# Kernel tuning notes

Hardware: AMD Instinct MI355X
Metric: run time of the kernel (lower is better)

The kernel has to match this reference:

```python
import jax, jax.numpy as jnp
import numpy as np

N_NODES = 100000


def gcn_conv(x, W, b, src, dst, ew, n):
    """PyG GCNConv with edge_weight: add self-loops (weight 1), symmetric norm,
    linear transform, scatter-add aggregation, bias."""
    h = x @ W                                   # [N, F_out]
    # degree includes the self-loop weight of 1 per node
    deg = jnp.zeros((n,), dtype=x.dtype).at[dst].add(ew) + 1.0
    dinv = jax.lax.rsqrt(deg)                   # deg > 0 always (self-loop)
    norm = dinv[src] * ew * dinv[dst]           # [E]
    agg = jax.ops.segment_sum(h[src] * norm[:, None], dst, num_segments=n)
    # self-loop contribution: norm_ii = dinv[i]^2 * 1
    agg = agg + h * (dinv * dinv)[:, None]
    return agg + b


def setup_inputs() -> dict:
    key = jax.random.key(0)
    ks = jax.random.split(key, 9)
    N, E, F_in, F_h, F_out = N_NODES, 1600000, 128, 64, 10
    x = jax.random.normal(ks[0], (N, F_in), dtype=jnp.float32)
    edge_index = jax.random.randint(ks[1], (2, E), 0, N, dtype=jnp.int64)
    edge_weight = jax.random.uniform(ks[2], (E,), dtype=jnp.float32)
    def glorot(k, fi, fo):
        s = jnp.sqrt(6.0 / (fi + fo))
        return jax.random.uniform(k, (fi, fo), minval=-s, maxval=s, dtype=jnp.float32)
    return {
        "x": x,
        "edge_index": edge_index,
        "edge_weight": edge_weight,
        "W1": glorot(ks[3], F_in, F_h), "b1": jnp.zeros((F_h,), jnp.float32),
        "W2": glorot(ks[4], F_h, F_h), "b2": jnp.zeros((F_h,), jnp.float32),
        "Wfc": glorot(ks[5], F_h, F_out), "bfc": jnp.zeros((F_out,), jnp.float32),
    }


def reference(x, edge_index, edge_weight, W1, b1, W2, b2, Wfc, bfc):
    n = x.shape[0]
    src, dst = edge_index[0], edge_index[1]
    h = gcn_conv(x, W1, b1, src, dst, edge_weight, n)
    h = jax.nn.relu(h)
    h = gcn_conv(h, W2, b2, src, dst, edge_weight, n)
    h = jax.nn.relu(h)
    return h @ Wfc + bfc
```

## Files before the change

kernel.cpp:

```cpp
#include <hip/hip_runtime.h>

static constexpr int F_IN  = 128;
static constexpr int F_H   = 64;
static constexpr int F_OUT = 10;

static constexpr int NPB_SHIFT = 9;
static constexpr int NPB = 1 << NPB_SHIFT;
static constexpr int MAXC = 256;
static constexpr int EPB = 2048;

__device__ __forceinline__ unsigned short f2bf(float f) {
    unsigned u = __float_as_uint(f);
    return (unsigned short)((u + 0x7fff + ((u >> 16) & 1)) >> 16);
}
__device__ __forceinline__ float bf_lo(unsigned u) { return __uint_as_float(u << 16); }
__device__ __forceinline__ float bf_hi(unsigned u) { return __uint_as_float(u & 0xffff0000u); }

__global__ __launch_bounds__(64) void k_detect(const unsigned long long* __restrict__ u,
                                               int* __restrict__ flag) {
    unsigned long long v = u[threadIdx.x];
    int hz = ((v >> 32) == 0ull) ? 1 : 0;
    int all64 = __all(hz);
    if (threadIdx.x == 0) flag[0] = all64;
}

__device__ __forceinline__ int load_idx(const void* ein, bool f64, long i) {
    return f64 ? (int)((const long long*)ein)[i] : ((const int*)ein)[i];
}

__global__ __launch_bounds__(256) void k_part1(const void* __restrict__ ein,
                                               const float* __restrict__ ew,
                                               const int* __restrict__ flag,
                                               int* __restrict__ gcur,
                                               unsigned long long* __restrict__ packed,
                                               int E, int NC, int cap) {
    __shared__ int lcnt[MAXC];
    __shared__ int lofs[MAXC];
    int tid = threadIdx.x;
    if (tid < NC) lcnt[tid] = 0;
    __syncthreads();
    bool f = flag[0];
    int base = blockIdx.x * EPB;
#pragma unroll
    for (int j = 0; j < EPB / 256; ++j) {
        int e = base + j * 256 + tid;
        if (e < E) {
            int d = load_idx(ein, f, (long)E + e);
            atomicAdd(&lcnt[d >> NPB_SHIFT], 1);
        }
    }
    __syncthreads();
    if (tid < NC) {
        int c = lcnt[tid];
        lofs[tid] = c ? atomicAdd(&gcur[tid], c) : 0;
        lcnt[tid] = 0;
    }
    __syncthreads();
#pragma unroll
    for (int j = 0; j < EPB / 256; ++j) {
        int e = base + j * 256 + tid;
        if (e < E) {
            int s = load_idx(ein, f, e);
            int d = load_idx(ein, f, (long)E + e);
            unsigned int wb = __float_as_uint(ew[e]);
            int b = d >> NPB_SHIFT;
            int pos = lofs[b] + atomicAdd(&lcnt[b], 1);
            if (pos < cap) {
                unsigned long long u = (unsigned long long)wb
                                     | ((unsigned long long)(unsigned)s << 32)
                                     | ((unsigned long long)(unsigned)(d & (NPB - 1)) << 49);
                packed[(long)b * cap + pos] = u;
            }
        }
    }
}

__global__ __launch_bounds__(256) void k_chist(const unsigned long long* __restrict__ packed,
                                               const int* __restrict__ gcur,
                                               int* __restrict__ rp,
                                               int* __restrict__ pbt,
                                               float* __restrict__ dinv,
                                               int N, int cap) {
    __shared__ int   lc[NPB];
    __shared__ float ld[NPB];
    __shared__ int   sm[256];
    int b = blockIdx.x, tid = threadIdx.x;
#pragma unroll
    for (int i = tid; i < NPB; i += 256) { lc[i] = 0; ld[i] = 0.0f; }
    __syncthreads();
    int cnt = gcur[b];
    const unsigned long long* pk = packed + (long)b * cap;
    for (int p = tid; p < cnt; p += 256) {
        unsigned long long u = pk[p];
        int dl = (int)(u >> 49);
        atomicAdd(&lc[dl], 1);
        atomicAdd(&ld[dl], __uint_as_float((unsigned int)u));
    }
    __syncthreads();
    int c0 = lc[tid * 2], c1 = lc[tid * 2 + 1];
    int p0 = (c0 + 15) & ~15, p1 = (c1 + 15) & ~15;
    int s = p0 + p1;
    sm[tid] = s;
    __syncthreads();
    for (int off = 1; off < 256; off <<= 1) {
        int v = 0;
        if (tid >= off) v = sm[tid - off];
        __syncthreads();
        sm[tid] += v;
        __syncthreads();
    }
    int excl = sm[tid] - s;
    int n0 = b << NPB_SHIFT;
    int node0 = n0 + tid * 2, node1 = node0 + 1;
    if (node0 < N) {
        rp[node0]   = excl;
        dinv[node0] = rsqrtf(ld[tid * 2] + 1.0f);
    }
    if (node1 < N) {
        rp[node1]   = excl + p0;
        dinv[node1] = rsqrtf(ld[tid * 2 + 1] + 1.0f);
    }
    if (tid == 255) pbt[b] = sm[255];
}

__global__ __launch_bounds__(256) void k_scanP(const int* __restrict__ pbt,
                                               int* __restrict__ pbase,
                                               int* __restrict__ rp, int NC, int N) {
    __shared__ int sm[256];
    int tid = threadIdx.x;
    int c = (tid < NC) ? pbt[tid] : 0;
    sm[tid] = c;
    __syncthreads();
    for (int off = 1; off < 256; off <<= 1) {
        int v = 0;
        if (tid >= off) v = sm[tid - off];
        __syncthreads();
        sm[tid] += v;
        __syncthreads();
    }
    if (tid < NC) pbase[tid] = sm[tid] - c;
    if (tid == 255) rp[N] = sm[255];
}

__global__ __launch_bounds__(256) void k_rpfix(int* __restrict__ rp,
                                               const int* __restrict__ pbase, int N) {
    int i = blockIdx.x * 256 + threadIdx.x;
    if (i < N) rp[i] += pbase[i >> NPB_SHIFT];
}

__global__ __launch_bounds__(256) void k_cscatter(const unsigned long long* __restrict__ packed,
                                                  const int* __restrict__ gcur,
                                                  const int* __restrict__ rp,
                                                  const float* __restrict__ dinv,
                                                  uint2* __restrict__ recs,
                                                  int N, int cap) {
    __shared__ int   cur[NPB];
    __shared__ float dd[NPB];
    int b = blockIdx.x, tid = threadIdx.x;
    int n0 = b << NPB_SHIFT;
#pragma unroll
    for (int i = tid; i < NPB; i += 256) {
        int node = n0 + i;
        cur[i] = (node < N) ? rp[node]   : 0;
        dd[i]  = (node < N) ? dinv[node] : 0.0f;
    }
    __syncthreads();
    int cnt = gcur[b];
    const unsigned long long* pk = packed + (long)b * cap;
    for (int p = tid; p < cnt; p += 256) {
        unsigned long long u = pk[p];
        int dl = (int)(u >> 49);
        int s  = (int)((u >> 32) & 0x1FFFF);
        float w = __uint_as_float((unsigned int)u);
        int pos = atomicAdd(&cur[dl], 1);
        uint2 r;
        r.x = (unsigned)(s << 7);
        r.y = __float_as_uint(dinv[s] * w * dd[dl]);
        recs[pos] = r;
    }
    __syncthreads();
    for (int i = tid; i < NPB; i += 256) {
        int node = n0 + i;
        if (node < N) {
            int end = rp[node + 1];
            for (int p = cur[i]; p < end; ++p) recs[p] = make_uint2(0u, 0u);
        }
    }
}

template <int K>
__global__ __launch_bounds__(256) void k_gemm(const float* __restrict__ A,
                                              const float* __restrict__ W,
                                              unsigned short* __restrict__ Cb, int M) {
    __shared__ float As[128][32];
    __shared__ float Ws[32][64];
    int tid = threadIdx.x;
    int tx = tid & 15;
    int ty = tid >> 4;
    int rb = blockIdx.x * 128;
    float acc[8][4] = {};
    for (int kc = 0; kc < K; kc += 32) {
        __syncthreads();
#pragma unroll
        for (int i = 0; i < 4; ++i) {
            int e = tid + i * 256;
            int r = e >> 3, g = e & 7;
            int gr = rb + r;
            float4 v = make_float4(0.f, 0.f, 0.f, 0.f);
            if (gr < M) v = *(const float4*)&A[(long)gr * K + kc + g * 4];
            int gs = g ^ ((r >> 3) & 7);
            *(float4*)&As[r][gs * 4] = v;
        }
#pragma unroll
        for (int i = 0; i < 2; ++i) {
            int e = tid + i * 256;
            int k = e >> 4, n4 = e & 15;
            *(float4*)&Ws[k][n4 * 4] = *(const float4*)&W[(long)(kc + k) * 64 + n4 * 4];
        }
        __syncthreads();
#pragma unroll
        for (int g = 0; g < 8; ++g) {
            float4 b0 = *(const float4*)&Ws[g * 4 + 0][tx * 4];
            float4 b1 = *(const float4*)&Ws[g * 4 + 1][tx * 4];
            float4 b2 = *(const float4*)&Ws[g * 4 + 2][tx * 4];
            float4 b3 = *(const float4*)&Ws[g * 4 + 3][tx * 4];
            int gs = (g ^ (ty & 7)) * 4;
#pragma unroll
            for (int rr = 0; rr < 8; ++rr) {
                float4 a = *(const float4*)&As[ty * 8 + rr][gs];
                acc[rr][0] = fmaf(a.x, b0.x, acc[rr][0]);
                acc[rr][1] = fmaf(a.x, b0.y, acc[rr][1]);
                acc[rr][2] = fmaf(a.x, b0.z, acc[rr][2]);
                acc[rr][3] = fmaf(a.x, b0.w, acc[rr][3]);
                acc[rr][0] = fmaf(a.y, b1.x, acc[rr][0]);
                acc[rr][1] = fmaf(a.y, b1.y, acc[rr][1]);
                acc[rr][2] = fmaf(a.y, b1.z, acc[rr][2]);
                acc[rr][3] = fmaf(a.y, b1.w, acc[rr][3]);
                acc[rr][0] = fmaf(a.z, b2.x, acc[rr][0]);
                acc[rr][1] = fmaf(a.z, b2.y, acc[rr][1]);
                acc[rr][2] = fmaf(a.z, b2.z, acc[rr][2]);
                acc[rr][3] = fmaf(a.z, b2.w, acc[rr][3]);
                acc[rr][0] = fmaf(a.w, b3.x, acc[rr][0]);
                acc[rr][1] = fmaf(a.w, b3.y, acc[rr][1]);
                acc[rr][2] = fmaf(a.w, b3.z, acc[rr][2]);
                acc[rr][3] = fmaf(a.w, b3.w, acc[rr][3]);
            }
        }
    }
#pragma unroll
    for (int rr = 0; rr < 8; ++rr) {
        int gr = rb + ty * 8 + rr;
        if (gr < M) {
            ushort4 v;
            v.x = f2bf(acc[rr][0]); v.y = f2bf(acc[rr][1]);
            v.z = f2bf(acc[rr][2]); v.w = f2bf(acc[rr][3]);
            *(ushort4*)&Cb[(long)gr * 64 + tx * 4] = v;
        }
    }
}

__global__ __launch_bounds__(256, 4) void k_agg(const unsigned short* __restrict__ hb,
                                                const int* __restrict__ rp,
                                                const uint2* __restrict__ recs,
                                                const float* __restrict__ dinv,
                                                const float* __restrict__ bias,
                                                float* __restrict__ out, int N) {
    int wid  = (blockIdx.x * 256 + threadIdx.x) >> 6;
    int lane = threadIdx.x & 63;
    int fg   = lane & 15;
    int es   = lane >> 4;
    if (wid >= N) return;
    int fg8 = fg * 8;
    const char* hbase = (const char*)hb;
    int p0 = rp[wid], p1 = rp[wid + 1];
    float a0 = 0.f, a1 = 0.f, a2 = 0.f, a3 = 0.f;
    for (int pb = p0 + es * 4; pb < p1; pb += 16) {
        uint4 r01 = *(const uint4*)&recs[pb];
        uint4 r23 = *(const uint4*)&recs[pb + 2];
        uint2 h0 = *(const uint2*)(hbase + r01.x + fg8);
        uint2 h1 = *(const uint2*)(hbase + r01.z + fg8);
        uint2 h2 = *(const uint2*)(hbase + r23.x + fg8);
        uint2 h3 = *(const uint2*)(hbase + r23.z + fg8);
        float w0 = __uint_as_float(r01.y), w1 = __uint_as_float(r01.w);
        float w2 = __uint_as_float(r23.y), w3 = __uint_as_float(r23.w);
        a0 = fmaf(w0, bf_lo(h0.x), a0); a1 = fmaf(w0, bf_hi(h0.x), a1);
        a2 = fmaf(w0, bf_lo(h0.y), a2); a3 = fmaf(w0, bf_hi(h0.y), a3);
        a0 = fmaf(w1, bf_lo(h1.x), a0); a1 = fmaf(w1, bf_hi(h1.x), a1);
        a2 = fmaf(w1, bf_lo(h1.y), a2); a3 = fmaf(w1, bf_hi(h1.y), a3);
        a0 = fmaf(w2, bf_lo(h2.x), a0); a1 = fmaf(w2, bf_hi(h2.x), a1);
        a2 = fmaf(w2, bf_lo(h2.y), a2); a3 = fmaf(w2, bf_hi(h2.y), a3);
        a0 = fmaf(w3, bf_lo(h3.x), a0); a1 = fmaf(w3, bf_hi(h3.x), a1);
        a2 = fmaf(w3, bf_lo(h3.y), a2); a3 = fmaf(w3, bf_hi(h3.y), a3);
    }
#pragma unroll
    for (int m = 16; m <= 32; m <<= 1) {
        a0 += __shfl_xor(a0, m);
        a1 += __shfl_xor(a1, m);
        a2 += __shfl_xor(a2, m);
        a3 += __shfl_xor(a3, m);
    }
    float di  = dinv[wid];
    float di2 = di * di;
    uint2 hs = *(const uint2*)(hbase + ((long)wid << 7) + fg8);
    float4 bv = *(const float4*)&bias[fg * 4];
    a0 = fmaf(bf_lo(hs.x), di2, a0 + bv.x);
    a1 = fmaf(bf_hi(hs.x), di2, a1 + bv.y);
    a2 = fmaf(bf_lo(hs.y), di2, a2 + bv.z);
    a3 = fmaf(bf_hi(hs.y), di2, a3 + bv.w);
    if (es == 0) {
        float4 r = make_float4(fmaxf(a0, 0.f), fmaxf(a1, 0.f),
                               fmaxf(a2, 0.f), fmaxf(a3, 0.f));
        *(float4*)&out[(long)wid * 64 + fg * 4] = r;
    }
}

__global__ __launch_bounds__(256) void k_fc(const float* __restrict__ h,
                                            const float* __restrict__ W,
                                            const float* __restrict__ b,
                                            float* __restrict__ out, int N) {
    __shared__ float Ws[64 * 10];
    __shared__ float bs[16];
    int tid = threadIdx.x;
    for (int e = tid; e < 64 * 10; e += 256) Ws[e] = W[e];
    if (tid < 10) bs[tid] = b[tid];
    __syncthreads();
    int i = blockIdx.x * 256 + tid;
    if (i >= N) return;
    float acc[10];
#pragma unroll
    for (int j = 0; j < 10; ++j) acc[j] = bs[j];
    const float4* row = (const float4*)&h[(long)i * 64];
#pragma unroll
    for (int c = 0; c < 16; ++c) {
        float4 a = row[c];
#pragma unroll
        for (int j = 0; j < 10; ++j) {
            acc[j] = fmaf(a.x, Ws[(4 * c + 0) * 10 + j], acc[j]);
            acc[j] = fmaf(a.y, Ws[(4 * c + 1) * 10 + j], acc[j]);
            acc[j] = fmaf(a.z, Ws[(4 * c + 2) * 10 + j], acc[j]);
            acc[j] = fmaf(a.w, Ws[(4 * c + 3) * 10 + j], acc[j]);
        }
    }
#pragma unroll
    for (int j = 0; j < 10; ++j) out[(long)i * 10 + j] = acc[j];
}

extern "C" void kernel_launch(void* const* d_in, const int* in_sizes, int n_in,
                              void* d_out, int out_size, void* d_ws, size_t ws_size,
                              hipStream_t stream) {
    const float* x    = (const float*)d_in[0];
    const void*  eidx = d_in[1];
    const float* ew   = (const float*)d_in[2];
    const float* W1   = (const float*)d_in[3];
    const float* b1   = (const float*)d_in[4];
    const float* W2   = (const float*)d_in[5];
    const float* b2   = (const float*)d_in[6];
    const float* Wfc  = (const float*)d_in[7];
    const float* bfc  = (const float*)d_in[8];
    float* out = (float*)d_out;

    const int N  = in_sizes[0] / F_IN;
    const int E  = in_sizes[2];
    const int NC = (N + NPB - 1) >> NPB_SHIFT;
    const int cap = E / NC + E / (8 * NC) + 1024;

    char* w = (char*)d_ws;
    size_t off = 0;
    auto alloc = [&](size_t bytes) {
        void* p = w + off;
        off += (bytes + 255) & ~(size_t)255;
        return p;
    };
    float* dinv  = (float*)alloc((size_t)N * 4);
    int*   rp    = (int*)alloc((size_t)(N + 1) * 4);
    int*   flag  = (int*)alloc(256);
    int*   gcur  = (int*)alloc((size_t)MAXC * 4);
    int*   pbt   = (int*)alloc((size_t)MAXC * 4);
    int*   pbase = (int*)alloc((size_t)MAXC * 4);
    unsigned long long* packed =
        (unsigned long long*)alloc((size_t)NC * cap * 8);
    uint2* recs  = (uint2*)alloc(((size_t)E + 15u * (size_t)N + 64) * 8);
    unsigned short* h1b = (unsigned short*)alloc((size_t)N * F_H * 2);
    float* g1    = (float*)alloc((size_t)N * F_H * 4);
    unsigned short* h2b = h1b;
    float* g2    = g1;
    (void)ws_size;

    hipMemsetAsync(gcur, 0, (size_t)NC * 4, stream);

    const int PB = (E + EPB - 1) / EPB;

    k_detect<<<1, 64, 0, stream>>>((const unsigned long long*)eidx, flag);
    k_part1<<<PB, 256, 0, stream>>>(eidx, ew, flag, gcur, packed, E, NC, cap);
    k_chist<<<NC, 256, 0, stream>>>(packed, gcur, rp, pbt, dinv, N, cap);
    k_scanP<<<1, 256, 0, stream>>>(pbt, pbase, rp, NC, N);
    k_rpfix<<<(N + 255) / 256, 256, 0, stream>>>(rp, pbase, N);
    k_cscatter<<<NC, 256, 0, stream>>>(packed, gcur, rp, dinv, recs, N, cap);

    const int GB = (N + 127) / 128;
    k_gemm<F_IN><<<GB, 256, 0, stream>>>(x, W1, h1b, N);
    k_agg<<<(N + 3) / 4, 256, 0, stream>>>(h1b, rp, recs, dinv, b1, g1, N);
    k_gemm<F_H><<<GB, 256, 0, stream>>>(g1, W2, h2b, N);
    k_agg<<<(N + 3) / 4, 256, 0, stream>>>(h2b, rp, recs, dinv, b2, g2, N);
    k_fc<<<(N + 255) / 256, 256, 0, stream>>>(g2, Wfc, bfc, out, N);
}
```

Before: 220.5 us.

## Fuse FC into second aggregation, drop rpfix and memset, pad edges to 8

Fuses the final 64x10 linear layer into the second aggregation kernel, avoiding a full write and re-read of the hidden activations. Removes the rp fix-up kernel by adding per-chunk base offsets where rp is read, and folds the gcur zeroing into the detect kernel. Edge lists are padded to multiples of 8 instead of 16, and aggregation lanes now gather 16-byte feature chunks across 8 edge slots. EPB is doubled for the partition pass. The costs are extra pbase loads and redundant per-lane FC weight reads in the aggregation.

```diff
diff --git a/kernel.cpp b/kernel.cpp
--- a/kernel.cpp
+++ b/kernel.cpp
@@ -7,7 +7,7 @@
 static constexpr int NPB_SHIFT = 9;
 static constexpr int NPB = 1 << NPB_SHIFT;
 static constexpr int MAXC = 256;
-static constexpr int EPB = 2048;
+static constexpr int EPB = 4096;
 
 __device__ __forceinline__ unsigned short f2bf(float f) {
     unsigned u = __float_as_uint(f);
@@ -16,16 +16,21 @@
 __device__ __forceinline__ float bf_lo(unsigned u) { return __uint_as_float(u << 16); }
 __device__ __forceinline__ float bf_hi(unsigned u) { return __uint_as_float(u & 0xffff0000u); }
 
-__global__ __launch_bounds__(64) void k_detect(const unsigned long long* __restrict__ u,
-                                               int* __restrict__ flag) {
-    unsigned long long v = u[threadIdx.x];
-    int hz = ((v >> 32) == 0ull) ? 1 : 0;
-    int all64 = __all(hz);
-    if (threadIdx.x == 0) flag[0] = all64;
-}
-
 __device__ __forceinline__ int load_idx(const void* ein, bool f64, long i) {
     return f64 ? (int)((const long long*)ein)[i] : ((const int*)ein)[i];
+}
+
+__global__ __launch_bounds__(256) void k_detect_init(const unsigned long long* __restrict__ u,
+                                                     int* __restrict__ flag,
+                                                     int* __restrict__ gcur) {
+    int tid = threadIdx.x;
+    if (tid < MAXC) gcur[tid] = 0;
+    if (tid < 64) {
+        unsigned long long v = u[tid];
+        int hz = ((v >> 32) == 0ull) ? 1 : 0;
+        int all64 = __all(hz);
+        if (tid == 0) flag[0] = all64;
+    }
 }
 
 __global__ __launch_bounds__(256) void k_part1(const void* __restrict__ ein,
@@ -98,8 +103,8 @@
     }
     __syncthreads();
     int c0 = lc[tid * 2], c1 = lc[tid * 2 + 1];
-    int p0 = (c0 + 15) & ~15, p1 = (c1 + 15) & ~15;
-    int s = p0 + p1;
+    int pp0 = (c0 + 7) & ~7, pp1 = (c1 + 7) & ~7;
+    int s = pp0 + pp1;
     sm[tid] = s;
     __syncthreads();
     for (int off = 1; off < 256; off <<= 1) {
@@ -117,7 +122,7 @@
         dinv[node0] = rsqrtf(ld[tid * 2] + 1.0f);
     }
     if (node1 < N) {
-        rp[node1]   = excl + p0;
+        rp[node1]   = excl + pp0;
         dinv[node1] = rsqrtf(ld[tid * 2 + 1] + 1.0f);
     }
     if (tid == 255) pbt[b] = sm[255];
@@ -139,18 +144,14 @@
         __syncthreads();
     }
     if (tid < NC) pbase[tid] = sm[tid] - c;
-    if (tid == 255) rp[N] = sm[255];
-}
-
-__global__ __launch_bounds__(256) void k_rpfix(int* __restrict__ rp,
-                                               const int* __restrict__ pbase, int N) {
-    int i = blockIdx.x * 256 + threadIdx.x;
-    if (i < N) rp[i] += pbase[i >> NPB_SHIFT];
+    if (tid == NC - 1) rp[N] = c;
 }
 
 __global__ __launch_bounds__(256) void k_cscatter(const unsigned long long* __restrict__ packed,
                                                   const int* __restrict__ gcur,
                                                   const int* __restrict__ rp,
+                                                  const int* __restrict__ pbase,
+                                                  const int* __restrict__ pbt,
                                                   const float* __restrict__ dinv,
                                                   uint2* __restrict__ recs,
                                                   int N, int cap) {
@@ -158,11 +159,12 @@
     __shared__ float dd[NPB];
     int b = blockIdx.x, tid = threadIdx.x;
     int n0 = b << NPB_SHIFT;
+    int pb_ = pbase[b];
 #pragma unroll
     for (int i = tid; i < NPB; i += 256) {
         int node = n0 + i;
-        cur[i] = (node < N) ? rp[node]   : 0;
-        dd[i]  = (node < N) ? dinv[node] : 0.0f;
+        cur[i] = (node < N) ? rp[node] + pb_ : 0;
+        dd[i]  = (node < N) ? dinv[node]     : 0.0f;
     }
     __syncthreads();
     int cnt = gcur[b];
@@ -182,7 +184,8 @@
     for (int i = tid; i < NPB; i += 256) {
         int node = n0 + i;
         if (node < N) {
-            int end = rp[node + 1];
+            int el = (i == NPB - 1) ? pbt[b] : rp[node + 1];
+            int end = el + pb_;
             for (int p = cur[i]; p < end; ++p) recs[p] = make_uint2(0u, 0u);
         }
     }
@@ -259,90 +262,102 @@
     }
 }
 
+template <bool FC>
 __global__ __launch_bounds__(256, 4) void k_agg(const unsigned short* __restrict__ hb,
                                                 const int* __restrict__ rp,
+                                                const int* __restrict__ pbase,
                                                 const uint2* __restrict__ recs,
                                                 const float* __restrict__ dinv,
                                                 const float* __restrict__ bias,
-                                                float* __restrict__ out, int N) {
+                                                const float* __restrict__ Wfc,
+                                                const float* __restrict__ bfc,
+                                                float* __restrict__ out,
+                                                int N, int NC) {
     int wid  = (blockIdx.x * 256 + threadIdx.x) >> 6;
     int lane = threadIdx.x & 63;
-    int fg   = lane & 15;
-    int es   = lane >> 4;
+    int fg   = lane & 7;
+    int es   = lane >> 3;
     if (wid >= N) return;
-    int fg8 = fg * 8;
     const char* hbase = (const char*)hb;
-    int p0 = rp[wid], p1 = rp[wid + 1];
+    int p0 = rp[wid] + pbase[wid >> NPB_SHIFT];
+    int b1 = (wid + 1) >> NPB_SHIFT;
+    if (b1 >= NC) b1 = NC - 1;
+    int p1 = rp[wid + 1] + pbase[b1];
+    int fg16 = fg * 16;
     float a0 = 0.f, a1 = 0.f, a2 = 0.f, a3 = 0.f;
-    for (int pb = p0 + es * 4; pb < p1; pb += 16) {
-        uint4 r01 = *(const uint4*)&recs[pb];
-        uint4 r23 = *(const uint4*)&recs[pb + 2];
-        uint2 h0 = *(const uint2*)(hbase + r01.x + fg8);
-        uint2 h1 = *(const uint2*)(hbase + r01.z + fg8);
-        uint2 h2 = *(const uint2*)(hbase + r23.x + fg8);
-        uint2 h3 = *(const uint2*)(hbase + r23.z + fg8);
-        float w0 = __uint_as_float(r01.y), w1 = __uint_as_float(r01.w);
-        float w2 = __uint_as_float(r23.y), w3 = __uint_as_float(r23.w);
-        a0 = fmaf(w0, bf_lo(h0.x), a0); a1 = fmaf(w0, bf_hi(h0.x), a1);
-        a2 = fmaf(w0, bf_lo(h0.y), a2); a3 = fmaf(w0, bf_hi(h0.y), a3);
-        a0 = fmaf(w1, bf_lo(h1.x), a0); a1 = fmaf(w1, bf_hi(h1.x), a1);
-        a2 = fmaf(w1, bf_lo(h1.y), a2); a3 = fmaf(w1, bf_hi(h1.y), a3);
-        a0 = fmaf(w2, bf_lo(h2.x), a0); a1 = fmaf(w2, bf_hi(h2.x), a1);
-        a2 = fmaf(w2, bf_lo(h2.y), a2); a3 = fmaf(w2, bf_hi(h2.y), a3);
-        a0 = fmaf(w3, bf_lo(h3.x), a0); a1 = fmaf(w3, bf_hi(h3.x), a1);
-        a2 = fmaf(w3, bf_lo(h3.y), a2); a3 = fmaf(w3, bf_hi(h3.y), a3);
-    }
-#pragma unroll
-    for (int m = 16; m <= 32; m <<= 1) {
-        a0 += __shfl_xor(a0, m);
-        a1 += __shfl_xor(a1, m);
-        a2 += __shfl_xor(a2, m);
-        a3 += __shfl_xor(a3, m);
+    float a4 = 0.f, a5 = 0.f, a6 = 0.f, a7 = 0.f;
+    for (int pb = p0 + es; pb < p1; pb += 8) {
+        uint2 rc = recs[pb];
+        uint4 hv = *(const uint4*)(hbase + rc.x + fg16);
+        float w  = __uint_as_float(rc.y);
+        a0 = fmaf(w, bf_lo(hv.x), a0); a1 = fmaf(w, bf_hi(hv.x), a1);
+        a2 = fmaf(w, bf_lo(hv.y), a2); a3 = fmaf(w, bf_hi(hv.y), a3);
+        a4 = fmaf(w, bf_lo(hv.z), a4); a5 = fmaf(w, bf_hi(hv.z), a5);
+        a6 = fmaf(w, bf_lo(hv.w), a6); a7 = fmaf(w, bf_hi(hv.w), a7);
+    }
+#pragma unroll
+    for (int m = 8; m <= 32; m <<= 1) {
+        a0 += __shfl_xor(a0, m); a1 += __shfl_xor(a1, m);
+        a2 += __shfl_xor(a2, m); a3 += __shfl_xor(a3, m);
+        a4 += __shfl_xor(a4, m); a5 += __shfl_xor(a5, m);
+        a6 += __shfl_xor(a6, m); a7 += __shfl_xor(a7, m);
     }
     float di  = dinv[wid];
     float di2 = di * di;
-    uint2 hs = *(const uint2*)(hbase + ((long)wid << 7) + fg8);
-    float4 bv = *(const float4*)&bias[fg * 4];
-    a0 = fmaf(bf_lo(hs.x), di2, a0 + bv.x);
-    a1 = fmaf(bf_hi(hs.x), di2, a1 + bv.y);
-    a2 = fmaf(bf_lo(hs.y), di2, a2 + bv.z);
-    a3 = fmaf(bf_hi(hs.y), di2, a3 + bv.w);
-    if (es == 0) {
-        float4 r = make_float4(fmaxf(a0, 0.f), fmaxf(a1, 0.f),
-                               fmaxf(a2, 0.f), fmaxf(a3, 0.f));
-        *(float4*)&out[(long)wid * 64 + fg * 4] = r;
-    }
-}
-
-__global__ __launch_bounds__(256) void k_fc(const float* __restrict__ h,
-                                            const float* __restrict__ W,
-                                            const float* __restrict__ b,
-                                            float* __restrict__ out, int N) {
-    __shared__ float Ws[64 * 10];
-    __shared__ float bs[16];
-    int tid = threadIdx.x;
-    for (int e = tid; e < 64 * 10; e += 256) Ws[e] = W[e];
-    if (tid < 10) bs[tid] = b[tid];
-    __syncthreads();
-    int i = blockIdx.x * 256 + tid;
-    if (i >= N) return;
-    float acc[10];
-#pragma unroll
-    for (int j = 0; j < 10; ++j) acc[j] = bs[j];
-    const float4* row = (const float4*)&h[(long)i * 64];
-#pragma unroll
-    for (int c = 0; c < 16; ++c) {
-        float4 a = row[c];
+    uint4 hs = *(const uint4*)(hbase + ((long)wid << 7) + fg16);
+    float4 bv0 = *(const float4*)&bias[fg * 8];
+    float4 bv1 = *(const float4*)&bias[fg * 8 + 4];
+    a0 = fmaf(bf_lo(hs.x), di2, a0 + bv0.x);
+    a1 = fmaf(bf_hi(hs.x), di2, a1 + bv0.y);
+    a2 = fmaf(bf_lo(hs.y), di2, a2 + bv0.z);
+    a3 = fmaf(bf_hi(hs.y), di2, a3 + bv0.w);
+    a4 = fmaf(bf_lo(hs.z), di2, a4 + bv1.x);
+    a5 = fmaf(bf_hi(hs.z), di2, a5 + bv1.y);
+    a6 = fmaf(bf_lo(hs.w), di2, a6 + bv1.z);
+    a7 = fmaf(bf_hi(hs.w), di2, a7 + bv1.w);
+    float r0 = fmaxf(a0, 0.f), r1 = fmaxf(a1, 0.f);
+    float r2 = fmaxf(a2, 0.f), r3 = fmaxf(a3, 0.f);
+    float r4 = fmaxf(a4, 0.f), r5 = fmaxf(a5, 0.f);
+    float r6 = fmaxf(a6, 0.f), r7 = fmaxf(a7, 0.f);
+    if (!FC) {
+        if (es == 0) {
+            *(float4*)&out[(long)wid * 64 + fg * 8]     = make_float4(r0, r1, r2, r3);
+            *(float4*)&out[(long)wid * 64 + fg * 8 + 4] = make_float4(r4, r5, r6, r7);
+        }
+    } else {
+        float p[10];
+#pragma unroll
+        for (int j = 0; j < 10; ++j) p[j] = 0.f;
+        float rr[8] = {r0, r1, r2, r3, r4, r5, r6, r7};
+#pragma unroll
+        for (int t = 0; t < 8; ++t) {
+            const float* wr = &Wfc[(fg * 8 + t) * 10];
+            float2 w01 = *(const float2*)&wr[0];
+            float2 w23 = *(const float2*)&wr[2];
+            float2 w45 = *(const float2*)&wr[4];
+            float2 w67 = *(const float2*)&wr[6];
+            float2 w89 = *(const float2*)&wr[8];
+            p[0] = fmaf(rr[t], w01.x, p[0]); p[1] = fmaf(rr[t], w01.y, p[1]);
+            p[2] = fmaf(rr[t], w23.x, p[2]); p[3] = fmaf(rr[t], w23.y, p[3]);
+            p[4] = fmaf(rr[t], w45.x, p[4]); p[5] = fmaf(rr[t], w45.y, p[5]);
+            p[6] = fmaf(rr[t], w67.x, p[6]); p[7] = fmaf(rr[t], w67.y, p[7]);
+            p[8] = fmaf(rr[t], w89.x, p[8]); p[9] = fmaf(rr[t], w89.y, p[9]);
+        }
 #pragma unroll
         for (int j = 0; j < 10; ++j) {
-            acc[j] = fmaf(a.x, Ws[(4 * c + 0) * 10 + j], acc[j]);
-            acc[j] = fmaf(a.y, Ws[(4 * c + 1) * 10 + j], acc[j]);
-            acc[j] = fmaf(a.z, Ws[(4 * c + 2) * 10 + j], acc[j]);
-            acc[j] = fmaf(a.w, Ws[(4 * c + 3) * 10 + j], acc[j]);
-        }
-    }
-#pragma unroll
-    for (int j = 0; j < 10; ++j) out[(long)i * 10 + j] = acc[j];
+            p[j] += __shfl_xor(p[j], 1);
+            p[j] += __shfl_xor(p[j], 2);
+            p[j] += __shfl_xor(p[j], 4);
+            p[j] += bfc[j];
+        }
+        if (lane == 0) {
+            *(float2*)&out[(long)wid * 10 + 0] = make_float2(p[0], p[1]);
+            *(float2*)&out[(long)wid * 10 + 2] = make_float2(p[2], p[3]);
+            *(float2*)&out[(long)wid * 10 + 4] = make_float2(p[4], p[5]);
+            *(float2*)&out[(long)wid * 10 + 6] = make_float2(p[6], p[7]);
+            *(float2*)&out[(long)wid * 10 + 8] = make_float2(p[8], p[9]);
+        }
+    }
 }
 
 extern "C" void kernel_launch(void* const* d_in, const int* in_sizes, int n_in,
@@ -379,28 +394,25 @@
     int*   pbase = (int*)alloc((size_t)MAXC * 4);
     unsigned long long* packed =
         (unsigned long long*)alloc((size_t)NC * cap * 8);
-    uint2* recs  = (uint2*)alloc(((size_t)E + 15u * (size_t)N + 64) * 8);
+    uint2* recs  = (uint2*)alloc(((size_t)E + 7u * (size_t)N + 64) * 8);
     unsigned short* h1b = (unsigned short*)alloc((size_t)N * F_H * 2);
     float* g1    = (float*)alloc((size_t)N * F_H * 4);
     unsigned short* h2b = h1b;
-    float* g2    = g1;
     (void)ws_size;
 
-    hipMemsetAsync(gcur, 0, (size_t)NC * 4, stream);
-
     const int PB = (E + EPB - 1) / EPB;
 
-    k_detect<<<1, 64, 0, stream>>>((const unsigned long long*)eidx, flag);
+    k_detect_init<<<1, 256, 0, stream>>>((const unsigned long long*)eidx, flag, gcur);
     k_part1<<<PB, 256, 0, stream>>>(eidx, ew, flag, gcur, packed, E, NC, cap);
     k_chist<<<NC, 256, 0, stream>>>(packed, gcur, rp, pbt, dinv, N, cap);
     k_scanP<<<1, 256, 0, stream>>>(pbt, pbase, rp, NC, N);
-    k_rpfix<<<(N + 255) / 256, 256, 0, stream>>>(rp, pbase, N);
-    k_cscatter<<<NC, 256, 0, stream>>>(packed, gcur, rp, dinv, recs, N, cap);
+    k_cscatter<<<NC, 256, 0, stream>>>(packed, gcur, rp, pbase, pbt, dinv, recs, N, cap);
 
     const int GB = (N + 127) / 128;
     k_gemm<F_IN><<<GB, 256, 0, stream>>>(x, W1, h1b, N);
-    k_agg<<<(N + 3) / 4, 256, 0, stream>>>(h1b, rp, recs, dinv, b1, g1, N);
+    k_agg<false><<<(N + 3) / 4, 256, 0, stream>>>(h1b, rp, pbase, recs, dinv, b1,
+                                                  nullptr, nullptr, g1, N, NC);
     k_gemm<F_H><<<GB, 256, 0, stream>>>(g1, W2, h2b, N);
-    k_agg<<<(N + 3) / 4, 256, 0, stream>>>(h2b, rp, recs, dinv, b2, g2, N);
-    k_fc<<<(N + 255) / 256, 256, 0, stream>>>(g2, Wfc, bfc, out, N);
-}
+    k_agg<true><<<(N + 3) / 4, 256, 0, stream>>>(h2b, rp, pbase, recs, dinv, b2,
+                                                 Wfc, bfc, out, N, NC);
+}
```

Result: slower. 324.2 us (+47.0%).
